# Kernel tuning notes

Hardware: AMD Instinct MI355X
Metric: run time of the kernel (lower is better)

## Reference

```python
import jax, jax.numpy as jnp
import numpy as np

B, S, E, H = 2, 2048, 1024, 16
D = E // H  # head_dim = 64
FE = 4      # forward_expansion
EPS = 1e-5


def layernorm(x, g, b):
    mu = jnp.mean(x, axis=-1, keepdims=True)
    var = jnp.var(x, axis=-1, keepdims=True)
    return (x - mu) * jax.lax.rsqrt(var + EPS) * g + b


def setup_inputs() -> dict:
    key = jax.random.key(0)
    ks = jax.random.split(key, 16)
    s = lambda d: 1.0 / np.sqrt(d)
    return {
        "queries": jax.random.normal(ks[0], (B, S, E), jnp.float32),
        "keys": jax.random.normal(ks[1], (B, S, E), jnp.float32),
        "values": jax.random.normal(ks[2], (B, S, E), jnp.float32),
        "mask": jnp.ones((B, 1, S, S), jnp.int32),  # ignored (faithful to source bug)
        "Wq": jax.random.normal(ks[3], (D, D), jnp.float32) * s(D),
        "Wk": jax.random.normal(ks[4], (D, D), jnp.float32) * s(D),
        "Wv": jax.random.normal(ks[5], (D, D), jnp.float32) * s(D),
        "Wfc": jax.random.normal(ks[6], (E, E), jnp.float32) * s(E),
        "bfc": jnp.zeros((E,), jnp.float32),
        "W1": jax.random.normal(ks[7], (FE * E, E), jnp.float32) * s(E),
        "b1": jnp.zeros((FE * E,), jnp.float32),
        "W2": jax.random.normal(ks[8], (E, FE * E), jnp.float32) * s(FE * E),
        "b2": jnp.zeros((E,), jnp.float32),
        "ln1_g": jnp.ones((E,), jnp.float32),
        "ln1_b": jnp.zeros((E,), jnp.float32),
        "ln2_g": jnp.ones((E,), jnp.float32),
        "ln2_b": jnp.zeros((E,), jnp.float32),
    }


def reference(queries, keys, values, mask, Wq, Wk, Wv, Wfc, bfc, W1, b1, W2, b2,
              ln1_g, ln1_b, ln2_g, ln2_b):
    # --- MHA ---
    q = queries.reshape(B, S, H, D) @ Wq.T  # [B,S,H,D]
    k = keys.reshape(B, S, H, D) @ Wk.T
    v = values.reshape(B, S, H, D) @ Wv.T
    scores = jnp.einsum('bqhd,bkhd->bhqk', q, k)
    # source: softmax(scores / S**(-1/2)) == scores * sqrt(S)  (faithful quirk)
    # mask is ignored: source masked_fill is non-inplace and discarded
    attn = jax.nn.softmax(scores * jnp.sqrt(jnp.float32(S)), axis=-1)
    out = jnp.einsum('bhqk,bkhd->bqhd', attn, v).reshape(B, S, E)
    att = out @ Wfc.T + bfc
    # --- residual + LN + FFN + LN (dropout p=0 -> identity) ---
    h = layernorm(att + queries, ln1_g, ln1_b)
    x = jax.nn.relu(h @ W1.T + b1) @ W2.T + b2
    return layernorm(x + h, ln2_g, ln2_b)
```

## Files before the change

kernel.cpp:

```cpp
#include <hip/hip_runtime.h>
#include <hip/hip_bf16.h>
#include <math.h>

#define B_ 2
#define S_ 2048
#define E_ 1024
#define H_ 16
#define D_ 64
#define TOK (B_*S_)
#define SCALE2 (45.254833995939045f * 1.44269504088896340f)

typedef __bf16 bf16x8 __attribute__((ext_vector_type(8)));
typedef float floatx4 __attribute__((ext_vector_type(4)));
struct b4s { __hip_bfloat16 x, y, z, w; };

typedef const __attribute__((address_space(1))) char ga_char;
typedef __attribute__((address_space(3))) char ls_char;

__device__ __forceinline__ void gload_lds16(const void* g, ls_char* l) {
  __builtin_amdgcn_global_load_lds((ga_char*)g, l, 16, 0, 0);
}

#if __has_builtin(__builtin_amdgcn_exp2f)
#define EXP2(x) __builtin_amdgcn_exp2f(x)
#else
#define EXP2(x) exp2f(x)
#endif

#define SWZ(arr, half, row, qpos) \
  (*(bf16x8*)&arr[half][row][(((qpos) ^ ((row) & 3)) * 8)])

__global__ __launch_bounds__(256) void cast_all(
    const float* __restrict__ Wfc, const float* __restrict__ W1,
    const float* __restrict__ W2, __hip_bfloat16* __restrict__ Wfcb,
    __hip_bfloat16* __restrict__ W1b, __hip_bfloat16* __restrict__ W2b,
    const float* __restrict__ Wq, const float* __restrict__ Wk,
    const float* __restrict__ Wv, __hip_bfloat16* __restrict__ Whl) {
  const int i = blockIdx.x * 256 + threadIdx.x;
  if (i < 2359296) {
    const float* src; __hip_bfloat16* dst; int j;
    if (i < 262144)       { src = Wfc; dst = Wfcb; j = i; }
    else if (i < 1310720) { src = W1;  dst = W1b;  j = i - 262144; }
    else                  { src = W2;  dst = W2b;  j = i - 1310720; }
    float4 v = ((const float4*)src)[j];
    b4s o;
    o.x = __float2bfloat16(v.x); o.y = __float2bfloat16(v.y);
    o.z = __float2bfloat16(v.z); o.w = __float2bfloat16(v.w);
    *(b4s*)(dst + (size_t)j * 4) = o;
  } else if (i < 2362368) {
    const int idx = i - 2359296;
    const int m = idx >> 10;
    const int off = (idx & 1023) * 4;
    const float* W = (m == 0) ? Wq : (m == 1) ? Wk : Wv;
    float4 v = *(const float4*)(W + off);
    b4s hi, lo;
    hi.x = __float2bfloat16(v.x); lo.x = __float2bfloat16(v.x - __bfloat162float(hi.x));
    hi.y = __float2bfloat16(v.y); lo.y = __float2bfloat16(v.y - __bfloat162float(hi.y));
    hi.z = __float2bfloat16(v.z); lo.z = __float2bfloat16(v.z - __bfloat162float(hi.z));
    hi.w = __float2bfloat16(v.w); lo.w = __float2bfloat16(v.w - __bfloat162float(hi.w));
    *(b4s*)(Whl + (size_t)m * 8192 + off) = hi;
    *(b4s*)(Whl + (size_t)m * 8192 + 4096 + off) = lo;
  }
}

__global__ __launch_bounds__(256) void qkv_fused(
    const float* __restrict__ xq, const float* __restrict__ xk,
    const float* __restrict__ xv, const __hip_bfloat16* __restrict__ Whl,
    __hip_bfloat16* __restrict__ qhi, __hip_bfloat16* __restrict__ qlo,
    __hip_bfloat16* __restrict__ khi, __hip_bfloat16* __restrict__ klo,
    __hip_bfloat16* __restrict__ vt) {
  __shared__ __bf16 Xh[2][64][32], Xl[2][64][32];
  __shared__ __bf16 Vt[64][72];
  const int t = threadIdx.x, lane = t & 63, w = t >> 6;
  const int quad = lane >> 4, low = lane & 15;
  const int bh = blockIdx.y;
  const int b = bh >> 4, h = bh & 15;
  const int s0 = blockIdx.x * 64;
  const int sr = t >> 2;
  const int sc = (t & 3) * 16;
  const int scc = sc >> 5;
  const int p0 = (sc & 31) >> 3;

  for (int m = 0; m < 3; m++) {
    const float* xin = (m == 0) ? xq : (m == 1) ? xk : xv;
    const __hip_bfloat16* Wh = Whl + (size_t)m * 8192;
    const float sc_m = (m == 0) ? SCALE2 : 1.0f;

    __syncthreads();
    {
      const float* src = xin + ((size_t)(b * S_ + s0 + sr)) * E_ + h * 64 + sc;
      float4 f0 = *(const float4*)(src);
      float4 f1 = *(const float4*)(src + 4);
      float4 f2 = *(const float4*)(src + 8);
      float4 f3 = *(const float4*)(src + 12);
      float fv[16] = {f0.x, f0.y, f0.z, f0.w, f1.x, f1.y, f1.z, f1.w,
                      f2.x, f2.y, f2.z, f2.w, f3.x, f3.y, f3.z, f3.w};
      bf16x8 hi0, hi1, lo0, lo1;
      #pragma unroll
      for (int j = 0; j < 8; j++) {
        hi0[j] = (__bf16)fv[j];
        lo0[j] = (__bf16)(fv[j] - (float)hi0[j]);
        hi1[j] = (__bf16)fv[8 + j];
        lo1[j] = (__bf16)(fv[8 + j] - (float)hi1[j]);
      }
      SWZ(Xh, scc, sr, p0) = hi0;
      SWZ(Xh, scc, sr, p0 + 1) = hi1;
      SWZ(Xl, scc, sr, p0) = lo0;
      SWZ(Xl, scc, sr, p0 + 1) = lo1;
    }
    __syncthreads();

    bf16x8 ah[2], al[2];
    #pragma unroll
    for (int c = 0; c < 2; c++) {
      ah[c] = SWZ(Xh, c, w * 16 + low, quad);
      al[c] = SWZ(Xl, c, w * 16 + low, quad);
    }

    floatx4 acc[4];
    #pragma unroll
    for (int nn = 0; nn < 4; nn++) {
      floatx4 a = {};
      #pragma unroll
      for (int c = 0; c < 2; c++) {
        const __hip_bfloat16* wp = Wh + (nn * 16 + low) * 64 + c * 32 + quad * 8;
        bf16x8 wh_ = *(const bf16x8*)wp;
        bf16x8 wl_ = *(const bf16x8*)(wp + 4096);
        a = __builtin_amdgcn_mfma_f32_16x16x32_bf16(ah[c], wh_, a, 0, 0, 0);
        a = __builtin_amdgcn_mfma_f32_16x16x32_bf16(al[c], wh_, a, 0, 0, 0);
        a = __builtin_amdgcn_mfma_f32_16x16x32_bf16(ah[c], wl_, a, 0, 0, 0);
      }
      acc[nn] = a;
    }

    if (m < 2) {
      __hip_bfloat16* dh = (m == 0) ? qhi : khi;
      __hip_bfloat16* dl = (m == 0) ? qlo : klo;
      #pragma unroll
      for (int nn = 0; nn < 4; nn++) {
        #pragma unroll
        for (int i = 0; i < 4; i++) {
          const int s = s0 + w * 16 + quad * 4 + i;
          const int d = nn * 16 + low;
          const size_t adr = ((size_t)bh * S_ + s) * 64 + d;
          const float f = acc[nn][i] * sc_m;
          const __hip_bfloat16 hb = __float2bfloat16(f);
          dh[adr] = hb;
          dl[adr] = __float2bfloat16(f - __bfloat162float(hb));
        }
      }
    } else {
      #pragma unroll
      for (int nn = 0; nn < 4; nn++)
        #pragma unroll
        for (int i = 0; i < 4; i++)
          Vt[nn * 16 + low][w * 16 + quad * 4 + i] = (__bf16)acc[nn][i];
      __syncthreads();
      const int dr = t >> 2;
      const int scl = (t & 3) * 16;
      __hip_bfloat16* dst = vt + ((size_t)bh * 64 + dr) * S_ + s0 + scl;
      bf16x8 o0 = *(const bf16x8*)&Vt[dr][scl];
      bf16x8 o1 = *(const bf16x8*)&Vt[dr][scl + 8];
      *(bf16x8*)dst = o0;
      *(bf16x8*)(dst + 8) = o1;
    }
  }
}

__device__ __forceinline__ void softmax_update(
    const floatx4* sa, floatx4* oacc, float& mrow, float& lrow, bf16x8* pb) {
  float rmax;
  {
    float m0 = fmaxf(fmaxf(sa[0][0], sa[0][1]), fmaxf(sa[0][2], sa[0][3]));
    float m1 = fmaxf(fmaxf(sa[1][0], sa[1][1]), fmaxf(sa[1][2], sa[1][3]));
    float m2 = fmaxf(fmaxf(sa[2][0], sa[2][1]), fmaxf(sa[2][2], sa[2][3]));
    float m3 = fmaxf(fmaxf(sa[3][0], sa[3][1]), fmaxf(sa[3][2], sa[3][3]));
    rmax = fmaxf(fmaxf(m0, m1), fmaxf(m2, m3));
    rmax = fmaxf(rmax, __shfl_xor(rmax, 16, 64));
    rmax = fmaxf(rmax, __shfl_xor(rmax, 32, 64));
  }
  if (__any(rmax > mrow)) {
    const float nm = fmaxf(mrow, rmax);
    const float al = EXP2(mrow - nm);
    mrow = nm;
    lrow *= al;
    #pragma unroll
    for (int dt = 0; dt < 4; dt++) {
      oacc[dt][0] *= al; oacc[dt][1] *= al;
      oacc[dt][2] *= al; oacc[dt][3] *= al;
    }
  }
  float p[4][4];
  float rs;
  {
    float r0_ = 0.f, r1_ = 0.f, r2_ = 0.f, r3_ = 0.f;
    #pragma unroll
    for (int i = 0; i < 4; i++) {
      p[0][i] = EXP2(sa[0][i] - mrow); r0_ += p[0][i];
      p[1][i] = EXP2(sa[1][i] - mrow); r1_ += p[1][i];
      p[2][i] = EXP2(sa[2][i] - mrow); r2_ += p[2][i];
      p[3][i] = EXP2(sa[3][i] - mrow); r3_ += p[3][i];
    }
    rs = (r0_ + r1_) + (r2_ + r3_);
    rs += __shfl_xor(rs, 16, 64);
    rs += __shfl_xor(rs, 32, 64);
  }
  lrow += rs;
  #pragma unroll
  for (int kh2 = 0; kh2 < 2; kh2++) {
    bf16x8 v;
    v[0] = (__bf16)p[kh2][0]; v[1] = (__bf16)p[kh2][1];
    v[2] = (__bf16)p[kh2][2]; v[3] = (__bf16)p[kh2][3];
    v[4] = (__bf16)p[kh2 + 2][0]; v[5] = (__bf16)p[kh2 + 2][1];
    v[6] = (__bf16)p[kh2 + 2][2]; v[7] = (__bf16)p[kh2 + 2][3];
    pb[kh2] = v;
  }
}

__global__ __launch_bounds__(512, 4) void attn_mfma(
    const __hip_bfloat16* __restrict__ Qhi, const __hip_bfloat16* __restrict__ Qlo,
    const __hip_bfloat16* __restrict__ Khi, const __hip_bfloat16* __restrict__ Klo,
    const __hip_bfloat16* __restrict__ Vtg, __hip_bfloat16* __restrict__ ctx) {
  __shared__ __bf16 Kh[2][2][64][32], Kl[2][2][64][32], Vs[2][2][64][32];
  const int t = threadIdx.x, lane = t & 63, w = t >> 6;
  const int quad = lane >> 4, low = lane & 15;
  const int bh = blockIdx.x;
  const int qw = blockIdx.y * 128 + w * 16;

  const int sh = w >> 2;
  const int r0 = (w & 3) * 16;
  const int srow = r0 + (lane >> 2);
  const int sq = (lane & 3) ^ (srow & 3);
  const __hip_bfloat16* gK = Khi + ((size_t)bh * S_ + srow) * 64 + sh * 32 + sq * 8;
  const __hip_bfloat16* gL = Klo + ((size_t)bh * S_ + srow) * 64 + sh * 32 + sq * 8;
  const __hip_bfloat16* gV = Vtg + ((size_t)bh * 64 + srow) * S_ + sh * 32 + sq * 8;

  bf16x8 qh[2], ql[2];
  {
    const size_t qbase = ((size_t)bh * S_ + qw + low) * 64 + quad * 8;
    qh[0] = *(const bf16x8*)(Qhi + qbase);
    qh[1] = *(const bf16x8*)(Qhi + qbase + 32);
    ql[0] = *(const bf16x8*)(Qlo + qbase);
    ql[1] = *(const bf16x8*)(Qlo + qbase + 32);
  }

  floatx4 oacc[4] = {};
  float mrow = -3e38f, lrow = 0.f;

  gload_lds16(gK, (ls_char*)&Kh[0][sh][r0][0]);
  gload_lds16(gL, (ls_char*)&Kl[0][sh][r0][0]);
  gload_lds16(gV, (ls_char*)&Vs[0][sh][r0][0]);

  for (int kt = 0; kt < S_ / 64; kt++) {
    const int cur = kt & 1;
    __syncthreads();
    if (kt + 1 < S_ / 64) {
      gload_lds16(gK + (size_t)(kt + 1) * 4096, (ls_char*)&Kh[cur ^ 1][sh][r0][0]);
      gload_lds16(gL + (size_t)(kt + 1) * 4096, (ls_char*)&Kl[cur ^ 1][sh][r0][0]);
      gload_lds16(gV + (size_t)(kt + 1) * 64,   (ls_char*)&Vs[cur ^ 1][sh][r0][0]);
    }

    floatx4 sa[4];
    __builtin_amdgcn_s_setprio(1);
    #pragma unroll
    for (int nn = 0; nn < 4; nn++) {
      const int prow = (nn & 1) * 32 + (nn >> 1) * 4 + (low >> 2) * 8 + (low & 3);
      bf16x8 kh0 = SWZ(Kh[cur], 0, prow, quad);
      bf16x8 kh1 = SWZ(Kh[cur], 1, prow, quad);
      bf16x8 kl0 = SWZ(Kl[cur], 0, prow, quad);
      bf16x8 kl1 = SWZ(Kl[cur], 1, prow, quad);
      floatx4 s = {};
      s = __builtin_amdgcn_mfma_f32_16x16x32_bf16(kh0, qh[0], s, 0, 0, 0);
      s = __builtin_amdgcn_mfma_f32_16x16x32_bf16(kh1, qh[1], s, 0, 0, 0);
      s = __builtin_amdgcn_mfma_f32_16x16x32_bf16(kl0, qh[0], s, 0, 0, 0);
      s = __builtin_amdgcn_mfma_f32_16x16x32_bf16(kl1, qh[1], s, 0, 0, 0);
      s = __builtin_amdgcn_mfma_f32_16x16x32_bf16(kh0, ql[0], s, 0, 0, 0);
      s = __builtin_amdgcn_mfma_f32_16x16x32_bf16(kh1, ql[1], s, 0, 0, 0);
      sa[nn] = s;
    }
    __builtin_amdgcn_s_setprio(0);

    bf16x8 pb[2];
    softmax_update(sa, oacc, mrow, lrow, pb);

    __builtin_amdgcn_s_setprio(1);
    #pragma unroll
    for (int dt = 0; dt < 4; dt++) {
      bf16x8 vb0 = SWZ(Vs[cur], 0, dt * 16 + low, quad);
      bf16x8 vb1 = SWZ(Vs[cur], 1, dt * 16 + low, quad);
      oacc[dt] = __builtin_amdgcn_mfma_f32_16x16x32_bf16(vb0, pb[0], oacc[dt], 0, 0, 0);
      oacc[dt] = __builtin_amdgcn_mfma_f32_16x16x32_bf16(vb1, pb[1], oacc[dt], 0, 0, 0);
    }
    __builtin_amdgcn_s_setprio(0);
  }

  const float inv = 1.0f / lrow;
  const int b = bh >> 4, h = bh & 15;
  const size_t base = ((size_t)(b * S_ + qw + low)) * E_ + h * 64 + quad * 4;
  #pragma unroll
  for (int dt = 0; dt < 4; dt++) {
    b4s o;
    o.x = __float2bfloat16(oacc[dt][0] * inv);
    o.y = __float2bfloat16(oacc[dt][1] * inv);
    o.z = __float2bfloat16(oacc[dt][2] * inv);
    o.w = __float2bfloat16(oacc[dt][3] * inv);
    *(b4s*)(ctx + base + dt * 16) = o;
  }
}

template <int RELU, int OUT_BF16, int PARTIAL>
__global__ __launch_bounds__(256) void gemm_mfma(
    const __hip_bfloat16* __restrict__ A, const __hip_bfloat16* __restrict__ Wt,
    const float* __restrict__ bias, void* __restrict__ C0, void* __restrict__ C1,
    int M, int N, int Kblk, int lda) {
  __shared__ __bf16 As[128][64];
  __shared__ __bf16 Bs[128][64];
  const int t = threadIdx.x;
  const int lane = t & 63;
  const int w = t >> 6;
  const int wr = w >> 1, wc = w & 1;
  const int m0 = blockIdx.y * 128, n0 = blockIdx.x * 128;
  void* Cout = (blockIdx.z == 0) ? C0 : C1;

  A += (size_t)blockIdx.z * Kblk;
  Wt += (size_t)blockIdx.z * Kblk;

  floatx4 acc[4][4] = {};
  const int srow = t >> 3;
  const int ssc = ((t & 7) ^ (srow & 7)) * 8;

  const __hip_bfloat16* gA = A + (size_t)(m0 + srow) * lda + ssc;
  const __hip_bfloat16* gB = Wt + (size_t)(n0 + srow) * lda + ssc;
  ls_char* lA = (ls_char*)&As[0][0] + w * 1024;
  ls_char* lB = (ls_char*)&Bs[0][0] + w * 1024;
  const size_t rstep = (size_t)32 * lda;

  for (int k0 = 0; k0 < Kblk; k0 += 64) {
    __syncthreads();
    gload_lds16(gA + k0,             lA);
    gload_lds16(gA + k0 + rstep,     lA + 4096);
    gload_lds16(gA + k0 + 2 * rstep, lA + 8192);
    gload_lds16(gA + k0 + 3 * rstep, lA + 12288);
    gload_lds16(gB + k0,             lB);
    gload_lds16(gB + k0 + rstep,     lB + 4096);
    gload_lds16(gB + k0 + 2 * rstep, lB + 8192);
    gload_lds16(gB + k0 + 3 * rstep, lB + 12288);
    __syncthreads();

    #pragma unroll
    for (int ks = 0; ks < 2; ks++) {
      bf16x8 af[4], bfr[4];
      #pragma unroll
      for (int i = 0; i < 4; i++) {
        const int ra = wr * 64 + i * 16 + (lane & 15);
        const int ca = (((lane >> 4) + ks * 4) ^ (ra & 7)) * 8;
        af[i] = *(const bf16x8*)&As[ra][ca];
        const int rb = wc * 64 + i * 16 + (lane & 15);
        const int cb = (((lane >> 4) + ks * 4) ^ (rb & 7)) * 8;
        bfr[i] = *(const bf16x8*)&Bs[rb][cb];
      }
      #pragma unroll
      for (int mi = 0; mi < 4; mi++)
        #pragma unroll
        for (int ni = 0; ni < 4; ni++)
          acc[mi][ni] = __builtin_amdgcn_mfma_f32_16x16x32_bf16(
              af[mi], bfr[ni], acc[mi][ni], 0, 0, 0);
    }
  }

  const int cil = lane & 15;
  const int quad = lane >> 4;
  #pragma unroll
  for (int ni = 0; ni < 4; ni++) {
    const int col = n0 + wc * 64 + ni * 16 + cil;
    const float bb = PARTIAL ? 0.f : bias[col];
    #pragma unroll
    for (int mi = 0; mi < 4; mi++) {
      const int row = m0 + wr * 64 + mi * 16 + quad * 4;
      #pragma unroll
      for (int i = 0; i < 4; i++) {
        if (PARTIAL) {
          ((float*)Cout)[(size_t)(row + i) * N + col] = acc[mi][ni][i];
        } else {
          float vv = acc[mi][ni][i] + bb;
          if (RELU) vv = fmaxf(vv, 0.f);
          if (OUT_BF16)
            ((__hip_bfloat16*)Cout)[(size_t)(row + i) * N + col] = __float2bfloat16(vv);
          else
            ((float*)Cout)[(size_t)(row + i) * N + col] = vv;
        }
      }
    }
  }
}

template <int EMIT_BF16, int HAS_A1, int HAS_BIAS>
__global__ __launch_bounds__(256) void add_ln(
    const float* __restrict__ a0, const float* __restrict__ a1,
    const float* __restrict__ r, const float* __restrict__ bias,
    const float* __restrict__ g, const float* __restrict__ bt,
    float* __restrict__ out, __hip_bfloat16* __restrict__ outb) {
  __shared__ float red[16];
  const int tok = blockIdx.x, t = threadIdx.x;
  float4 av = ((const float4*)(a0 + (size_t)tok * E_))[t];
  float4 rv = ((const float4*)(r + (size_t)tok * E_))[t];
  float4 x;
  x.x = av.x + rv.x; x.y = av.y + rv.y; x.z = av.z + rv.z; x.w = av.w + rv.w;
  if (HAS_A1) {
    float4 a2 = ((const float4*)(a1 + (size_t)tok * E_))[t];
    x.x += a2.x; x.y += a2.y; x.z += a2.z; x.w += a2.w;
  }
  if (HAS_BIAS) {
    float4 cv = ((const float4*)bias)[t];
    x.x += cv.x; x.y += cv.y; x.z += cv.z; x.w += cv.w;
  }
  float sum = x.x + x.y + x.z + x.w;
  float ssq = x.x * x.x + x.y * x.y + x.z * x.z + x.w * x.w;
  #pragma unroll
  for (int off = 32; off >= 1; off >>= 1) {
    sum += __shfl_down(sum, off, 64);
    ssq += __shfl_down(ssq, off, 64);
  }
  const int wave = t >> 6;
  if ((t & 63) == 0) { red[wave] = sum; red[4 + wave] = ssq; }
  __syncthreads();
  if (t == 0) {
    float s = red[0] + red[1] + red[2] + red[3];
    float qq = red[4] + red[5] + red[6] + red[7];
    float mu = s * (1.0f / E_);
    red[8] = mu;
    red[9] = qq * (1.0f / E_) - mu * mu;
  }
  __syncthreads();
  const float mu = red[8];
  const float inv = rsqrtf(red[9] + 1e-5f);
  float4 gv = ((const float4*)g)[t];
  float4 bv = ((const float4*)bt)[t];
  float4 o;
  o.x = (x.x - mu) * inv * gv.x + bv.x;
  o.y = (x.y - mu) * inv * gv.y + bv.y;
  o.z = (x.z - mu) * inv * gv.z + bv.z;
  o.w = (x.w - mu) * inv * gv.w + bv.w;
  ((float4*)(out + (size_t)tok * E_))[t] = o;
  if (EMIT_BF16) {
    b4s ob;
    ob.x = __float2bfloat16(o.x); ob.y = __float2bfloat16(o.y);
    ob.z = __float2bfloat16(o.z); ob.w = __float2bfloat16(o.w);
    *(b4s*)(outb + (size_t)tok * E_ + t * 4) = ob;
  }
}

extern "C" void kernel_launch(void* const* d_in, const int* in_sizes, int n_in,
                              void* d_out, int out_size, void* d_ws, size_t ws_size,
                              hipStream_t stream) {
  const float* queries = (const float*)d_in[0];
  const float* keys    = (const float*)d_in[1];
  const float* values  = (const float*)d_in[2];
  const float* Wq  = (const float*)d_in[4];
  const float* Wk  = (const float*)d_in[5];
  const float* Wv  = (const float*)d_in[6];
  const float* Wfc = (const float*)d_in[7];
  const float* bfc = (const float*)d_in[8];
  const float* W1  = (const float*)d_in[9];
  const float* b1  = (const float*)d_in[10];
  const float* W2  = (const float*)d_in[11];
  const float* b2  = (const float*)d_in[12];
  const float* ln1_g = (const float*)d_in[13];
  const float* ln1_b = (const float*)d_in[14];
  const float* ln2_g = (const float*)d_in[15];
  const float* ln2_b = (const float*)d_in[16];

  const size_t M1 = 1048576;
  float* ws = (float*)d_ws;
  float* P0  = ws;
  float* P1  = ws + 4 * M1;
  float* Hf  = ws + 8 * M1;
  __hip_bfloat16* bb = (__hip_bfloat16*)(ws + 12 * M1);
  __hip_bfloat16* CTXb = bb;
  __hip_bfloat16* Hb   = bb + 4 * M1;
  __hip_bfloat16* Wfcb = bb + 8 * M1;
  __hip_bfloat16* W1b  = bb + 9 * M1;
  __hip_bfloat16* W2b  = bb + 13 * M1;
  __hip_bfloat16* Qhi  = bb + 17 * M1;
  __hip_bfloat16* Qlo  = bb + 21 * M1;
  __hip_bfloat16* Khi  = bb + 25 * M1;
  __hip_bfloat16* Klo  = bb + 29 * M1;
  __hip_bfloat16* Vtb  = bb + 33 * M1;
  __hip_bfloat16* FF1b = bb + 17 * M1;
  __hip_bfloat16* Whlb = bb + 37 * M1;
  float* out = (float*)d_out;

  cast_all<<<9228, 256, 0, stream>>>(Wfc, W1, W2, Wfcb, W1b, W2b,
                                     Wq, Wk, Wv, Whlb);

  qkv_fused<<<dim3(S_ / 64, B_ * H_), 256, 0, stream>>>(
      queries, keys, values, Whlb, Qhi, Qlo, Khi, Klo, Vtb);
  attn_mfma<<<dim3(B_ * H_, S_ / 128), 512, 0, stream>>>(
      Qhi, Qlo, Khi, Klo, Vtb, CTXb);
  gemm_mfma<0, 0, 0><<<dim3(E_ / 128, TOK / 128, 1), 256, 0, stream>>>(
      CTXb, Wfcb, bfc, P0, nullptr, TOK, E_, E_, E_);
  add_ln<1, 0, 0><<<TOK, 256, 0, stream>>>(
      P0, nullptr, queries, nullptr, ln1_g, ln1_b, Hf, Hb);
  gemm_mfma<1, 1, 0><<<dim3(4 * E_ / 128, TOK / 128, 1), 256, 0, stream>>>(
      Hb, W1b, b1, FF1b, nullptr, TOK, 4 * E_, E_, E_);
  gemm_mfma<0, 0, 1><<<dim3(E_ / 128, TOK / 128, 2), 256, 0, stream>>>(
      FF1b, W2b, nullptr, P0, P1, TOK, E_, 2048, 4 * E_);
  add_ln<0, 1, 1><<<TOK, 256, 0, stream>>>(
      P0, P1, Hf, b2, ln2_g, ln2_b, out, nullptr);
}
```

Measured before the change: 399.7 us.

## Load attention K/V straight from global memory and split-K the output projection

The attention kernel drops its LDS double-buffered K/V staging and barriers. Each wave now reads its K and V fragments straight from global memory (relying on cache reuse), with 256-thread blocks covering 64 queries. Separately, the Wfc projection GEMM becomes a 2-way split-K writing two partials, and the bias add moves into the following add+layernorm kernel. This removes syncthreads and LDS traffic and adds parallelism to the projection, but it risks redundant global/L2 reads and uncoalesced strided loads of V in the attention loop.

```diff
diff --git a/kernel.cpp b/kernel.cpp
--- a/kernel.cpp
+++ b/kernel.cpp
@@ -217,23 +217,14 @@
   }
 }
 
-__global__ __launch_bounds__(512, 4) void attn_mfma(
+__global__ __launch_bounds__(256, 4) void attn_mfma(
     const __hip_bfloat16* __restrict__ Qhi, const __hip_bfloat16* __restrict__ Qlo,
     const __hip_bfloat16* __restrict__ Khi, const __hip_bfloat16* __restrict__ Klo,
     const __hip_bfloat16* __restrict__ Vtg, __hip_bfloat16* __restrict__ ctx) {
-  __shared__ __bf16 Kh[2][2][64][32], Kl[2][2][64][32], Vs[2][2][64][32];
   const int t = threadIdx.x, lane = t & 63, w = t >> 6;
   const int quad = lane >> 4, low = lane & 15;
   const int bh = blockIdx.x;
-  const int qw = blockIdx.y * 128 + w * 16;
-
-  const int sh = w >> 2;
-  const int r0 = (w & 3) * 16;
-  const int srow = r0 + (lane >> 2);
-  const int sq = (lane & 3) ^ (srow & 3);
-  const __hip_bfloat16* gK = Khi + ((size_t)bh * S_ + srow) * 64 + sh * 32 + sq * 8;
-  const __hip_bfloat16* gL = Klo + ((size_t)bh * S_ + srow) * 64 + sh * 32 + sq * 8;
-  const __hip_bfloat16* gV = Vtg + ((size_t)bh * 64 + srow) * S_ + sh * 32 + sq * 8;
+  const int qw = blockIdx.y * 64 + w * 16;
 
   bf16x8 qh[2], ql[2];
   {
@@ -244,31 +235,24 @@
     ql[1] = *(const bf16x8*)(Qlo + qbase + 32);
   }
 
+  const int prb = (low >> 2) * 8 + (low & 3);
+  const __hip_bfloat16* kh_p = Khi + ((size_t)bh * S_ + prb) * 64 + quad * 8;
+  const __hip_bfloat16* kl_p = Klo + ((size_t)bh * S_ + prb) * 64 + quad * 8;
+  const __hip_bfloat16* v_p  = Vtg + ((size_t)bh * 64 + low) * S_ + quad * 8;
+
   floatx4 oacc[4] = {};
   float mrow = -3e38f, lrow = 0.f;
 
-  gload_lds16(gK, (ls_char*)&Kh[0][sh][r0][0]);
-  gload_lds16(gL, (ls_char*)&Kl[0][sh][r0][0]);
-  gload_lds16(gV, (ls_char*)&Vs[0][sh][r0][0]);
-
   for (int kt = 0; kt < S_ / 64; kt++) {
-    const int cur = kt & 1;
-    __syncthreads();
-    if (kt + 1 < S_ / 64) {
-      gload_lds16(gK + (size_t)(kt + 1) * 4096, (ls_char*)&Kh[cur ^ 1][sh][r0][0]);
-      gload_lds16(gL + (size_t)(kt + 1) * 4096, (ls_char*)&Kl[cur ^ 1][sh][r0][0]);
-      gload_lds16(gV + (size_t)(kt + 1) * 64,   (ls_char*)&Vs[cur ^ 1][sh][r0][0]);
-    }
-
     floatx4 sa[4];
     __builtin_amdgcn_s_setprio(1);
     #pragma unroll
     for (int nn = 0; nn < 4; nn++) {
-      const int prow = (nn & 1) * 32 + (nn >> 1) * 4 + (low >> 2) * 8 + (low & 3);
-      bf16x8 kh0 = SWZ(Kh[cur], 0, prow, quad);
-      bf16x8 kh1 = SWZ(Kh[cur], 1, prow, quad);
-      bf16x8 kl0 = SWZ(Kl[cur], 0, prow, quad);
-      bf16x8 kl1 = SWZ(Kl[cur], 1, prow, quad);
+      const size_t ro = (size_t)kt * 4096 + (size_t)((nn & 1) * 32 + (nn >> 1) * 4) * 64;
+      bf16x8 kh0 = *(const bf16x8*)(kh_p + ro);
+      bf16x8 kh1 = *(const bf16x8*)(kh_p + ro + 32);
+      bf16x8 kl0 = *(const bf16x8*)(kl_p + ro);
+      bf16x8 kl1 = *(const bf16x8*)(kl_p + ro + 32);
       floatx4 s = {};
       s = __builtin_amdgcn_mfma_f32_16x16x32_bf16(kh0, qh[0], s, 0, 0, 0);
       s = __builtin_amdgcn_mfma_f32_16x16x32_bf16(kh1, qh[1], s, 0, 0, 0);
@@ -286,8 +270,9 @@
     __builtin_amdgcn_s_setprio(1);
     #pragma unroll
     for (int dt = 0; dt < 4; dt++) {
-      bf16x8 vb0 = SWZ(Vs[cur], 0, dt * 16 + low, quad);
-      bf16x8 vb1 = SWZ(Vs[cur], 1, dt * 16 + low, quad);
+      const size_t vo = (size_t)(dt * 16) * S_ + (size_t)kt * 64;
+      bf16x8 vb0 = *(const bf16x8*)(v_p + vo);
+      bf16x8 vb1 = *(const bf16x8*)(v_p + vo + 32);
       oacc[dt] = __builtin_amdgcn_mfma_f32_16x16x32_bf16(vb0, pb[0], oacc[dt], 0, 0, 0);
       oacc[dt] = __builtin_amdgcn_mfma_f32_16x16x32_bf16(vb1, pb[1], oacc[dt], 0, 0, 0);
     }
@@ -495,12 +480,12 @@
 
   qkv_fused<<<dim3(S_ / 64, B_ * H_), 256, 0, stream>>>(
       queries, keys, values, Whlb, Qhi, Qlo, Khi, Klo, Vtb);
-  attn_mfma<<<dim3(B_ * H_, S_ / 128), 512, 0, stream>>>(
+  attn_mfma<<<dim3(B_ * H_, S_ / 64), 256, 0, stream>>>(
       Qhi, Qlo, Khi, Klo, Vtb, CTXb);
-  gemm_mfma<0, 0, 0><<<dim3(E_ / 128, TOK / 128, 1), 256, 0, stream>>>(
-      CTXb, Wfcb, bfc, P0, nullptr, TOK, E_, E_, E_);
-  add_ln<1, 0, 0><<<TOK, 256, 0, stream>>>(
-      P0, nullptr, queries, nullptr, ln1_g, ln1_b, Hf, Hb);
+  gemm_mfma<0, 0, 1><<<dim3(E_ / 128, TOK / 128, 2), 256, 0, stream>>>(
+      CTXb, Wfcb, nullptr, P0, P1, TOK, E_, 512, E_);
+  add_ln<1, 1, 1><<<TOK, 256, 0, stream>>>(
+      P0, P1, queries, bfc, ln1_g, ln1_b, Hf, Hb);
   gemm_mfma<1, 1, 0><<<dim3(4 * E_ / 128, TOK / 128, 1), 256, 0, stream>>>(
       Hb, W1b, b1, FF1b, nullptr, TOK, 4 * E_, E_, E_);
   gemm_mfma<0, 0, 1><<<dim3(E_ / 128, TOK / 128, 2), 256, 0, stream>>>(
```

Result: slower. 654.2 us (+63.7%).

## Double-buffer GEMM LDS tiles and split-K the output projection

Applied to the files above, without the earlier changes.

The GEMM kernel now uses two LDS buffers and issues the global-to-LDS loads for the next K tile before computing the current one, dropping one barrier per iteration so memory traffic overlaps the MFMA work. The Wfc projection GEMM is also split into two K halves (grid z=2) writing partials, and the bias is added in the following add+layernorm kernel. This gives the small projection GEMM more blocks for occupancy, at the cost of doubled LDS per block and extra partial-buffer traffic. There is a possible hazard: the load into the other buffer is issued right after a single barrier, while other waves could still be reading that buffer from the previous step.

```diff
diff --git a/kernel.cpp b/kernel.cpp
--- a/kernel.cpp
+++ b/kernel.cpp
@@ -313,8 +313,8 @@
     const __hip_bfloat16* __restrict__ A, const __hip_bfloat16* __restrict__ Wt,
     const float* __restrict__ bias, void* __restrict__ C0, void* __restrict__ C1,
     int M, int N, int Kblk, int lda) {
-  __shared__ __bf16 As[128][64];
-  __shared__ __bf16 Bs[128][64];
+  __shared__ __bf16 As[2][128][64];
+  __shared__ __bf16 Bs[2][128][64];
   const int t = threadIdx.x;
   const int lane = t & 63;
   const int w = t >> 6;
@@ -331,21 +331,27 @@
 
   const __hip_bfloat16* gA = A + (size_t)(m0 + srow) * lda + ssc;
   const __hip_bfloat16* gB = Wt + (size_t)(n0 + srow) * lda + ssc;
-  ls_char* lA = (ls_char*)&As[0][0] + w * 1024;
-  ls_char* lB = (ls_char*)&Bs[0][0] + w * 1024;
   const size_t rstep = (size_t)32 * lda;
 
-  for (int k0 = 0; k0 < Kblk; k0 += 64) {
+#define GSTAGE(buf, k0) do {                                      \
+    ls_char* lA = (ls_char*)&As[buf][0][0] + w * 1024;            \
+    ls_char* lB = (ls_char*)&Bs[buf][0][0] + w * 1024;            \
+    gload_lds16(gA + (k0),             lA);                       \
+    gload_lds16(gA + (k0) + rstep,     lA + 4096);                \
+    gload_lds16(gA + (k0) + 2 * rstep, lA + 8192);                \
+    gload_lds16(gA + (k0) + 3 * rstep, lA + 12288);               \
+    gload_lds16(gB + (k0),             lB);                       \
+    gload_lds16(gB + (k0) + rstep,     lB + 4096);                \
+    gload_lds16(gB + (k0) + 2 * rstep, lB + 8192);                \
+    gload_lds16(gB + (k0) + 3 * rstep, lB + 12288);               \
+  } while (0)
+
+  GSTAGE(0, 0);
+  const int nsteps = Kblk >> 6;
+  for (int st = 0; st < nsteps; st++) {
+    const int cur = st & 1;
     __syncthreads();
-    gload_lds16(gA + k0,             lA);
-    gload_lds16(gA + k0 + rstep,     lA + 4096);
-    gload_lds16(gA + k0 + 2 * rstep, lA + 8192);
-    gload_lds16(gA + k0 + 3 * rstep, lA + 12288);
-    gload_lds16(gB + k0,             lB);
-    gload_lds16(gB + k0 + rstep,     lB + 4096);
-    gload_lds16(gB + k0 + 2 * rstep, lB + 8192);
-    gload_lds16(gB + k0 + 3 * rstep, lB + 12288);
-    __syncthreads();
+    if (st + 1 < nsteps) GSTAGE(cur ^ 1, (st + 1) * 64);
 
     #pragma unroll
     for (int ks = 0; ks < 2; ks++) {
@@ -354,10 +360,10 @@
       for (int i = 0; i < 4; i++) {
         const int ra = wr * 64 + i * 16 + (lane & 15);
         const int ca = (((lane >> 4) + ks * 4) ^ (ra & 7)) * 8;
-        af[i] = *(const bf16x8*)&As[ra][ca];
+        af[i] = *(const bf16x8*)&As[cur][ra][ca];
         const int rb = wc * 64 + i * 16 + (lane & 15);
         const int cb = (((lane >> 4) + ks * 4) ^ (rb & 7)) * 8;
-        bfr[i] = *(const bf16x8*)&Bs[rb][cb];
+        bfr[i] = *(const bf16x8*)&Bs[cur][rb][cb];
       }
       #pragma unroll
       for (int mi = 0; mi < 4; mi++)
@@ -367,6 +373,7 @@
               af[mi], bfr[ni], acc[mi][ni], 0, 0, 0);
     }
   }
+#undef GSTAGE
 
   const int cil = lane & 15;
   const int quad = lane >> 4;
@@ -497,10 +504,10 @@
       queries, keys, values, Whlb, Qhi, Qlo, Khi, Klo, Vtb);
   attn_mfma<<<dim3(B_ * H_, S_ / 128), 512, 0, stream>>>(
       Qhi, Qlo, Khi, Klo, Vtb, CTXb);
-  gemm_mfma<0, 0, 0><<<dim3(E_ / 128, TOK / 128, 1), 256, 0, stream>>>(
-      CTXb, Wfcb, bfc, P0, nullptr, TOK, E_, E_, E_);
-  add_ln<1, 0, 0><<<TOK, 256, 0, stream>>>(
-      P0, nullptr, queries, nullptr, ln1_g, ln1_b, Hf, Hb);
+  gemm_mfma<0, 0, 1><<<dim3(E_ / 128, TOK / 128, 2), 256, 0, stream>>>(
+      CTXb, Wfcb, nullptr, P0, P1, TOK, E_, 512, E_);
+  add_ln<1, 1, 1><<<TOK, 256, 0, stream>>>(
+      P0, P1, queries, bfc, ln1_g, ln1_b, Hf, Hb);
   gemm_mfma<1, 1, 0><<<dim3(4 * E_ / 128, TOK / 128, 1), 256, 0, stream>>>(
       Hb, W1b, b1, FF1b, nullptr, TOK, 4 * E_, E_, E_);
   gemm_mfma<0, 0, 1><<<dim3(E_ / 128, TOK / 128, 2), 256, 0, stream>>>(
```

After: 387.6 us. 1.03x faster.
